# Performance work log

Hardware: AMD Instinct MI355X
Metric: run time of the kernel (lower is better)

Reference implementation:

```python
import jax, jax.numpy as jnp
import numpy as np

TEMPERATURE = 0.1
EPS = 1e-12

def _l2norm(x):
    # matches F.normalize(x, dim=-1)
    return x / jnp.maximum(jnp.linalg.norm(x, axis=-1, keepdims=True), EPS)

def setup_inputs() -> dict:
    key = jax.random.key(0)
    k1, k2 = jax.random.split(key)
    N, D = 8192, 256
    images = jax.random.normal(k1, (N, D), dtype=jnp.float32)
    captions = jax.random.normal(k2, (N, D), dtype=jnp.float32)
    return {"images": images, "captions": captions}

def reference(images, captions):
    # Batched equivalent of the per-sample loop:
    # for each image i, InfoNCE(anchor=image_i, pos=caption_i, negs=all other captions)
    # and symmetrically for each caption. InfoNCE (unpaired mode) normalizes
    # embeddings, builds logits [pos, negs]/T, and applies CE with target 0.
    # Softmax is permutation-invariant, so this equals symmetric CE on the
    # full NxN similarity matrix with diagonal targets (CLIP loss).
    im = _l2norm(images)    # [N, D]
    cap = _l2norm(captions)  # [N, D]
    logits = jnp.einsum('id,jd->ij', im, cap) / TEMPERATURE  # [N, N]
    diag = jnp.arange(images.shape[0])
    # image->caption losses (rows), caption->image losses (columns)
    loss_i2c = -jax.nn.log_softmax(logits, axis=1)[diag, diag]
    loss_c2i = -jax.nn.log_softmax(logits, axis=0)[diag, diag]
    # original returns mean over the 2N concatenated per-sample losses
    return (jnp.mean(loss_i2c) + jnp.mean(loss_c2i)) * 0.5
```

## Files before the change

kernel.cpp:

```cpp
#include <hip/hip_runtime.h>
#include <hip/hip_bf16.h>

typedef short bf16x8 __attribute__((ext_vector_type(8)));
typedef float f32x4 __attribute__((ext_vector_type(4)));

typedef __attribute__((address_space(3))) void as3_void;
typedef const __attribute__((address_space(1))) void as1_void;

static constexpr int D = 256;
static constexpr float INV_T = 10.0f;

__device__ __forceinline__ ushort f2bf(float f) {
  union { float f; unsigned u; } v; v.f = f;
  unsigned r = v.u + 0x7fffu + ((v.u >> 16) & 1u);
  return (ushort)(r >> 16);
}

__global__ __launch_bounds__(256) void normalize_kernel(
    const float* __restrict__ im, const float* __restrict__ cap,
    ushort* __restrict__ imn, ushort* __restrict__ capn,
    float* __restrict__ diag, int N) {
  int tid = blockIdx.x * 256 + threadIdx.x;
  int w = tid >> 6;
  int lane = threadIdx.x & 63;
  if (w >= N) return;
  float4 vi = ((const float4*)(im + (size_t)w * D))[lane];
  float4 vc = ((const float4*)(cap + (size_t)w * D))[lane];
  float ssi = vi.x*vi.x + vi.y*vi.y + vi.z*vi.z + vi.w*vi.w;
  float ssc = vc.x*vc.x + vc.y*vc.y + vc.z*vc.z + vc.w*vc.w;
  #pragma unroll
  for (int m = 1; m < 64; m <<= 1) {
    ssi += __shfl_xor(ssi, m);
    ssc += __shfl_xor(ssc, m);
  }
  float ri = 1.0f / fmaxf(sqrtf(ssi), 1e-12f);
  float rc = 1.0f / fmaxf(sqrtf(ssc), 1e-12f);
  float ax = vi.x*ri, ay = vi.y*ri, az = vi.z*ri, aw = vi.w*ri;
  float cx = vc.x*rc, cy = vc.y*rc, cz = vc.z*rc, cw = vc.w*rc;
  ushort4 ua, uc;
  ua.x = f2bf(ax); ua.y = f2bf(ay); ua.z = f2bf(az); ua.w = f2bf(aw);
  uc.x = f2bf(cx); uc.y = f2bf(cy); uc.z = f2bf(cz); uc.w = f2bf(cw);
  ((ushort4*)(imn + (size_t)w * D))[lane] = ua;
  ((ushort4*)(capn + (size_t)w * D))[lane] = uc;
  float d = ax*cx + ay*cy + az*cz + aw*cw;
  #pragma unroll
  for (int m = 1; m < 64; m <<= 1) d += __shfl_xor(d, m);
  if (lane == 0) diag[w] = d * INV_T;
}

__global__ __launch_bounds__(512) void gemm_exp_kernel(
    const ushort* __restrict__ A, const ushort* __restrict__ Bm,
    float* __restrict__ rowpart, float* __restrict__ colpart, int N) {
  __shared__ ushort As[8][128 * 32];
  __shared__ ushort Bsh[8][2][64 * 32];
  int bm = blockIdx.x >> 2;
  int cg = blockIdx.x & 3;
  int tid = threadIdx.x;
  int lane = tid & 63;
  int wv = tid >> 6;
  int rb = lane & 15;
  int kb = (lane >> 4) * 8;
  int cc = kb ^ (((rb >> 1) & 3) * 8);

  int arow = tid >> 2;
  int ascol = 8 * ((tid & 3) ^ ((tid >> 3) & 3));
  const ushort* agS = A + ((size_t)bm * 128 + arow) * D + ascol;

  int su = 8 * ((lane & 3) ^ ((lane >> 3) & 3));
  const ushort* bgS = Bm + ((size_t)(wv * 64 + (lane >> 2))) * D + su;

  f32x4 acc[8][4];

#define VMWAIT(n) asm volatile("s_waitcnt vmcnt(" #n ")" ::: "memory")
#define LGKM0() asm volatile("s_waitcnt lgkmcnt(0)" ::: "memory")
#define BARRIER() asm volatile("s_barrier" ::: "memory")

#define STAGE_A(c)                                                           \
  __builtin_amdgcn_global_load_lds((as1_void*)(agS + (c) * 32),              \
      (as3_void*)(&As[c][tid * 8]), 16, 0, 0);

#define STAGE_B(P, T, KT) {                                                  \
    const ushort* bp = bgS + (size_t)(T) * 512 * D + (KT) * 32;              \
    _Pragma("unroll")                                                        \
    for (int i = 0; i < 4; ++i)                                              \
      __builtin_amdgcn_global_load_lds(                                      \
          (as1_void*)(bp + (size_t)i * 16 * D),                              \
          (as3_void*)(&Bsh[wv][P][i * 512 + lane * 8]), 16, 0, 0);           \
  }

#define READ_A(AF, KT)                                                      \
  { _Pragma("unroll") for (int mi = 0; mi < 8; ++mi)                        \
      AF[mi] = *(const bf16x8*)(&As[KT][(mi * 16 + rb) * 32 + cc]); }

#define READ_B(BF, P)                                                       \
  { _Pragma("unroll") for (int ni = 0; ni < 4; ++ni)                        \
      BF[ni] = *(const bf16x8*)(&Bsh[wv][P][(ni * 16 + rb) * 32 + cc]); }

#define MFMAS(AF, FB, CZ)                                                   \
  { __builtin_amdgcn_s_setprio(1);                                          \
    _Pragma("unroll") for (int mi = 0; mi < 8; ++mi)                        \
      _Pragma("unroll") for (int ni = 0; ni < 4; ++ni)                      \
        acc[mi][ni] = __builtin_amdgcn_mfma_f32_16x16x32_bf16(              \
            AF[mi], FB[ni],                                                 \
            (CZ) ? (f32x4){0.f, 0.f, 0.f, 0.f} : acc[mi][ni], 0, 0, 0);     \
    __builtin_amdgcn_s_setprio(0); }

#define EPILOGUE(T) {                                                         \
    _Pragma("unroll")                                                         \
    for (int mi = 0; mi < 8; ++mi)                                            \
      _Pragma("unroll")                                                       \
      for (int ni = 0; ni < 4; ++ni)                                          \
        _Pragma("unroll")                                                     \
        for (int r = 0; r < 4; ++r)                                           \
          acc[mi][ni][r] = __expf(acc[mi][ni][r] * INV_T);                    \
    bool sb0 = (lane & 1) != 0, sb1 = (lane & 2) != 0;                        \
    _Pragma("unroll")                                                         \
    for (int mi = 0; mi < 8; ++mi) {                                          \
      float v0 = acc[mi][0][0] + acc[mi][1][0] + acc[mi][2][0] + acc[mi][3][0]; \
      float v1 = acc[mi][0][1] + acc[mi][1][1] + acc[mi][2][1] + acc[mi][3][1]; \
      float v2 = acc[mi][0][2] + acc[mi][1][2] + acc[mi][2][2] + acc[mi][3][2]; \
      float v3 = acc[mi][0][3] + acc[mi][1][3] + acc[mi][2][3] + acc[mi][3][3]; \
      float h0 = (sb0 ? v1 : v0) + __shfl_xor(sb0 ? v0 : v1, 1);              \
      float h1 = (sb0 ? v3 : v2) + __shfl_xor(sb0 ? v2 : v3, 1);              \
      float g  = (sb1 ? h1 : h0) + __shfl_xor(sb1 ? h0 : h1, 2);              \
      g += __shfl_xor(g, 4);                                                  \
      g += __shfl_xor(g, 8);                                                  \
      if ((lane & 12) == 0)                                                   \
        rowpart[(size_t)((T) * 8 + wv) * N + bm * 128 + mi * 16 +             \
                (lane >> 4) * 4 + (lane & 3)] = g;                            \
    }                                                                         \
    _Pragma("unroll")                                                         \
    for (int ni = 0; ni < 4; ++ni) {                                          \
      float v = 0.f;                                                          \
      _Pragma("unroll")                                                       \
      for (int mi = 0; mi < 8; ++mi)                                          \
        _Pragma("unroll")                                                     \
        for (int r = 0; r < 4; ++r)                                           \
          v += acc[mi][ni][r];                                                \
      v += __shfl_xor(v, 16); v += __shfl_xor(v, 32);                         \
      if (lane < 16)                                                          \
        colpart[(size_t)bm * N + (T) * 512 + wv * 64 + ni * 16 + lane] = v;   \
    }                                                                         \
  }

  int T0 = cg * 4;
  STAGE_A(0) STAGE_A(1) STAGE_A(2) STAGE_A(3)
  STAGE_A(4) STAGE_A(5) STAGE_A(6) STAGE_A(7)
  STAGE_B(0, T0, 0)
  STAGE_B(1, T0, 1)
  VMWAIT(8);
  BARRIER();
  VMWAIT(4);
  bf16x8 fbA[4], fbB[4];
  READ_B(fbA, 0)

  for (int j = 0; j < 4; ++j) {
    int T = cg * 4 + j;
    bf16x8 af[8];
    LGKM0();
    READ_A(af, 0)
    if (j > 0) { VMWAIT(0); }
    STAGE_B(0, T, 2)
    if (j == 0) { VMWAIT(4); }
    READ_B(fbB, 1)
    MFMAS(af, fbA, 1)
    LGKM0(); STAGE_B(1, T, 3) READ_A(af, 1) VMWAIT(4); READ_B(fbA, 0)
    MFMAS(af, fbB, 0)
    LGKM0(); STAGE_B(0, T, 4) READ_A(af, 2) VMWAIT(4); READ_B(fbB, 1)
    MFMAS(af, fbA, 0)
    LGKM0(); STAGE_B(1, T, 5) READ_A(af, 3) VMWAIT(4); READ_B(fbA, 0)
    MFMAS(af, fbB, 0)
    LGKM0(); STAGE_B(0, T, 6) READ_A(af, 4) VMWAIT(4); READ_B(fbB, 1)
    MFMAS(af, fbA, 0)
    LGKM0(); STAGE_B(1, T, 7) READ_A(af, 5) VMWAIT(4); READ_B(fbA, 0)
    MFMAS(af, fbB, 0)
    LGKM0();
    if (j < 3) { STAGE_B(0, T + 1, 0) READ_A(af, 6) VMWAIT(4); }
    else       { READ_A(af, 6) VMWAIT(0); }
    READ_B(fbB, 1)
    MFMAS(af, fbA, 0)
    LGKM0();
    if (j < 3) { STAGE_B(1, T + 1, 1) READ_A(af, 7) VMWAIT(4); READ_B(fbA, 0) }
    else       { READ_A(af, 7) }
    MFMAS(af, fbB, 0)
    EPILOGUE(T)
  }
  VMWAIT(0);

#undef EPILOGUE
#undef MFMAS
#undef READ_B
#undef READ_A
#undef STAGE_B
#undef STAGE_A
#undef VMWAIT
#undef LGKM0
#undef BARRIER
}

__global__ __launch_bounds__(256) void reduce_kernel(
    const float* __restrict__ rowpart, const float* __restrict__ colpart,
    const float* __restrict__ diag, float* __restrict__ out,
    int N, int NPr, int NPc) {
  __shared__ float redr[4][64], redc[4][64];
  int w = threadIdx.x >> 6, s = threadIdx.x & 63;
  int i = blockIdx.x * 64 + s;
  float rs = 0.f, cs = 0.f;
  for (int k = w; k < NPr; k += 4) rs += rowpart[(size_t)k * N + i];
  for (int k = w; k < NPc; k += 4) cs += colpart[(size_t)k * N + i];
  redr[w][s] = rs; redc[w][s] = cs;
  __syncthreads();
  if (w == 0) {
    float R = redr[0][s] + redr[1][s] + redr[2][s] + redr[3][s];
    float C = redc[0][s] + redc[1][s] + redc[2][s] + redc[3][s];
    float l = logf(R) + logf(C) - 2.0f * diag[i];
    #pragma unroll
    for (int m = 1; m < 64; m <<= 1) l += __shfl_xor(l, m);
    if (s == 0) atomicAdd(out, l * (0.5f / (float)N));
  }
}

extern "C" void kernel_launch(void* const* d_in, const int* in_sizes, int n_in,
                              void* d_out, int out_size, void* d_ws, size_t ws_size,
                              hipStream_t stream) {
  const float* images = (const float*)d_in[0];
  const float* captions = (const float*)d_in[1];
  int N = in_sizes[0] / D;
  int NPr = 128;
  int NPc = 64;
  char* w = (char*)d_ws;
  size_t off = 0;
  ushort* imn  = (ushort*)(w + off); off += (size_t)N * D * 2;
  ushort* capn = (ushort*)(w + off); off += (size_t)N * D * 2;
  float* diag    = (float*)(w + off); off += (size_t)N * 4;
  float* rowpart = (float*)(w + off); off += (size_t)NPr * N * 4;
  float* colpart = (float*)(w + off); off += (size_t)NPc * N * 4;
  float* out = (float*)d_out;

  normalize_kernel<<<N / 4, 256, 0, stream>>>(images, captions, imn, capn, diag, N);
  gemm_exp_kernel<<<256, 512, 0, stream>>>(imn, capn, rowpart, colpart, N);
  hipMemsetAsync(out, 0, sizeof(float), stream);
  reduce_kernel<<<N / 64, 256, 0, stream>>>(rowpart, colpart, diag, out, N, NPr, NPc);
}
```

Measured before the change: 68.28 us.

## Shrink GEMM block tile to 64 rows and double grid for two blocks per CU

Halves the per-block A tile (128 to 64 rows) and per-wave B tile (64 to 32 columns), cutting accumulators from 32 to 8 MFMA tiles. Doubles the grid to 512 blocks with launch_bounds(512,2) so two blocks can co-reside per CU, which should hide latency better. The partial-sum buffers grow (256 row partials, 128 column partials), adding reduce work. Smaller tiles lower data reuse per MFMA, so LDS and global traffic per flop rises.

After: 82.61 us. 1.21x slower.

```diff
diff --git a/kernel.cpp b/kernel.cpp
--- a/kernel.cpp
+++ b/kernel.cpp
@@ -48,11 +48,11 @@
   if (lane == 0) diag[w] = d * INV_T;
 }
 
-__global__ __launch_bounds__(512) void gemm_exp_kernel(
+__global__ __launch_bounds__(512, 2) void gemm_exp_kernel(
     const ushort* __restrict__ A, const ushort* __restrict__ Bm,
     float* __restrict__ rowpart, float* __restrict__ colpart, int N) {
-  __shared__ ushort As[8][128 * 32];
-  __shared__ ushort Bsh[8][2][64 * 32];
+  __shared__ ushort As[8][64 * 32];
+  __shared__ ushort Bsh[8][2][32 * 32];
   int bm = blockIdx.x >> 2;
   int cg = blockIdx.x & 3;
   int tid = threadIdx.x;
@@ -62,44 +62,48 @@
   int kb = (lane >> 4) * 8;
   int cc = kb ^ (((rb >> 1) & 3) * 8);
 
-  int arow = tid >> 2;
-  int ascol = 8 * ((tid & 3) ^ ((tid >> 3) & 3));
-  const ushort* agS = A + ((size_t)bm * 128 + arow) * D + ascol;
+  int inner = tid & 255;
+  int chalf = tid >> 8;
+  int ar = inner >> 2;
+  int asu = 8 * ((inner & 3) ^ ((inner >> 3) & 3));
+  const ushort* agS = A + ((size_t)bm * 64 + ar) * D + asu;
 
   int su = 8 * ((lane & 3) ^ ((lane >> 3) & 3));
-  const ushort* bgS = Bm + ((size_t)(wv * 64 + (lane >> 2))) * D + su;
-
-  f32x4 acc[8][4];
+
+  f32x4 acc[4][2];
 
 #define VMWAIT(n) asm volatile("s_waitcnt vmcnt(" #n ")" ::: "memory")
 #define LGKM0() asm volatile("s_waitcnt lgkmcnt(0)" ::: "memory")
 #define BARRIER() asm volatile("s_barrier" ::: "memory")
 
-#define STAGE_A(c)                                                           \
-  __builtin_amdgcn_global_load_lds((as1_void*)(agS + (c) * 32),              \
-      (as3_void*)(&As[c][tid * 8]), 16, 0, 0);
+#define STAGE_A(r) {                                                         \
+    int c_ = chalf * 4 + (r);                                                \
+    __builtin_amdgcn_global_load_lds((as1_void*)(agS + c_ * 32),             \
+        (as3_void*)(&As[0][0] + c_ * 2048 + inner * 8), 16, 0, 0);           \
+  }
 
 #define STAGE_B(P, T, KT) {                                                  \
-    const ushort* bp = bgS + (size_t)(T) * 512 * D + (KT) * 32;              \
-    _Pragma("unroll")                                                        \
-    for (int i = 0; i < 4; ++i)                                              \
-      __builtin_amdgcn_global_load_lds(                                      \
-          (as1_void*)(bp + (size_t)i * 16 * D),                              \
-          (as3_void*)(&Bsh[wv][P][i * 512 + lane * 8]), 16, 0, 0);           \
+    const ushort* bp = Bm +                                                  \
+        ((size_t)(cg * 2048 + (T) * 256 + wv * 32 + (lane >> 2))) * D +      \
+        su + (KT) * 32;                                                      \
+    __builtin_amdgcn_global_load_lds((as1_void*)(bp),                        \
+        (as3_void*)(&Bsh[wv][P][lane * 8]), 16, 0, 0);                       \
+    __builtin_amdgcn_global_load_lds((as1_void*)(bp + (size_t)16 * D),       \
+        (as3_void*)(&Bsh[wv][P][512 + lane * 8]), 16, 0, 0);                 \
   }
 
 #define READ_A(AF, KT)                                                      \
-  { _Pragma("unroll") for (int mi = 0; mi < 8; ++mi)                        \
+  { _Pragma("unroll") for (int mi = 0; mi < 4; ++mi)                        \
       AF[mi] = *(const bf16x8*)(&As[KT][(mi * 16 + rb) * 32 + cc]); }
 
 #define READ_B(BF, P)                                                       \
-  { _Pragma("unroll") for (int ni = 0; ni < 4; ++ni)                        \
+  { _Pragma("unroll") for (int ni = 0; ni < 2; ++ni)                        \
       BF[ni] = *(const bf16x8*)(&Bsh[wv][P][(ni * 16 + rb) * 32 + cc]); }
 
 #define MFMAS(AF, FB, CZ)                                                   \
   { __builtin_amdgcn_s_setprio(1);                                          \
-    _Pragma("unroll") for (int mi = 0; mi < 8; ++mi)                        \
-      _Pragma("unroll") for (int ni = 0; ni < 4; ++ni)                      \
+    _Pragma("unroll") for (int mi = 0; mi < 4; ++mi)                        \
+      _Pragma("unroll") for (int ni = 0; ni < 2; ++ni)                      \
         acc[mi][ni] = __builtin_amdgcn_mfma_f32_16x16x32_bf16(              \
             AF[mi], FB[ni],                                                 \
             (CZ) ? (f32x4){0.f, 0.f, 0.f, 0.f} : acc[mi][ni], 0, 0, 0);     \
@@ -107,83 +111,78 @@
 
 #define EPILOGUE(T) {                                                         \
     _Pragma("unroll")                                                         \
-    for (int mi = 0; mi < 8; ++mi)                                            \
+    for (int mi = 0; mi < 4; ++mi)                                            \
       _Pragma("unroll")                                                       \
-      for (int ni = 0; ni < 4; ++ni)                                          \
+      for (int ni = 0; ni < 2; ++ni)                                          \
         _Pragma("unroll")                                                     \
         for (int r = 0; r < 4; ++r)                                           \
           acc[mi][ni][r] = __expf(acc[mi][ni][r] * INV_T);                    \
     bool sb0 = (lane & 1) != 0, sb1 = (lane & 2) != 0;                        \
     _Pragma("unroll")                                                         \
-    for (int mi = 0; mi < 8; ++mi) {                                          \
-      float v0 = acc[mi][0][0] + acc[mi][1][0] + acc[mi][2][0] + acc[mi][3][0]; \
-      float v1 = acc[mi][0][1] + acc[mi][1][1] + acc[mi][2][1] + acc[mi][3][1]; \
-      float v2 = acc[mi][0][2] + acc[mi][1][2] + acc[mi][2][2] + acc[mi][3][2]; \
-      float v3 = acc[mi][0][3] + acc[mi][1][3] + acc[mi][2][3] + acc[mi][3][3]; \
+    for (int mi = 0; mi < 4; ++mi) {                                          \
+      float v0 = acc[mi][0][0] + acc[mi][1][0];                               \
+      float v1 = acc[mi][0][1] + acc[mi][1][1];                               \
+      float v2 = acc[mi][0][2] + acc[mi][1][2];                               \
+      float v3 = acc[mi][0][3] + acc[mi][1][3];                               \
       float h0 = (sb0 ? v1 : v0) + __shfl_xor(sb0 ? v0 : v1, 1);              \
       float h1 = (sb0 ? v3 : v2) + __shfl_xor(sb0 ? v2 : v3, 1);              \
       float g  = (sb1 ? h1 : h0) + __shfl_xor(sb1 ? h0 : h1, 2);              \
       g += __shfl_xor(g, 4);                                                  \
       g += __shfl_xor(g, 8);                                                  \
       if ((lane & 12) == 0)                                                   \
-        rowpart[(size_t)((T) * 8 + wv) * N + bm * 128 + mi * 16 +             \
+        rowpart[(size_t)(cg * 64 + (T) * 8 + wv) * N + bm * 64 + mi * 16 +    \
                 (lane >> 4) * 4 + (lane & 3)] = g;                            \
     }                                                                         \
     _Pragma("unroll")                                                         \
-    for (int ni = 0; ni < 4; ++ni) {                                          \
+    for (int ni = 0; ni < 2; ++ni) {                                          \
       float v = 0.f;                                                          \
       _Pragma("unroll")                                                       \
-      for (int mi = 0; mi < 8; ++mi)                                          \
+      for (int mi = 0; mi < 4; ++mi)                                          \
         _Pragma("unroll")                                                     \
         for (int r = 0; r < 4; ++r)                                           \
           v += acc[mi][ni][r];                                                \
       v += __shfl_xor(v, 16); v += __shfl_xor(v, 32);                         \
       if (lane < 16)                                                          \
-        colpart[(size_t)bm * N + (T) * 512 + wv * 64 + ni * 16 + lane] = v;   \
+        colpart[(size_t)bm * N + cg * 2048 + (T) * 256 + wv * 32 + ni * 16 +  \
+                lane] = v;                                                    \
     }                                                                         \
   }
 
-  int T0 = cg * 4;
   STAGE_A(0) STAGE_A(1) STAGE_A(2) STAGE_A(3)
-  STAGE_A(4) STAGE_A(5) STAGE_A(6) STAGE_A(7)
-  STAGE_B(0, T0, 0)
-  STAGE_B(1, T0, 1)
-  VMWAIT(8);
+  STAGE_B(0, 0, 0)
+  STAGE_B(1, 0, 1)
+  VMWAIT(4);
   BARRIER();
-  VMWAIT(4);
-  bf16x8 fbA[4], fbB[4];
+  VMWAIT(2);
+  bf16x8 fbA[2], fbB[2];
   READ_B(fbA, 0)
 
-  for (int j = 0; j < 4; ++j) {
-    int T = cg * 4 + j;
-    bf16x8 af[8];
+  for (int T = 0; T < 8; ++T) {
+    bf16x8 af[4];
+    LGKM0(); STAGE_B(0, T, 2) READ_A(af, 0) VMWAIT(2); READ_B(fbB, 1)
+    MFMAS(af, fbA, 1)
+    LGKM0(); STAGE_B(1, T, 3) READ_A(af, 1) VMWAIT(2); READ_B(fbA, 0)
+    MFMAS(af, fbB, 0)
+    LGKM0(); STAGE_B(0, T, 4) READ_A(af, 2) VMWAIT(2); READ_B(fbB, 1)
+    MFMAS(af, fbA, 0)
+    LGKM0(); STAGE_B(1, T, 5) READ_A(af, 3) VMWAIT(2); READ_B(fbA, 0)
+    MFMAS(af, fbB, 0)
+    LGKM0(); STAGE_B(0, T, 6) READ_A(af, 4) VMWAIT(2); READ_B(fbB, 1)
+    MFMAS(af, fbA, 0)
+    LGKM0(); STAGE_B(1, T, 7) READ_A(af, 5) VMWAIT(2); READ_B(fbA, 0)
+    MFMAS(af, fbB, 0)
     LGKM0();
-    READ_A(af, 0)
-    if (j > 0) { VMWAIT(0); }
-    STAGE_B(0, T, 2)
-    if (j == 0) { VMWAIT(4); }
-    READ_B(fbB, 1)
-    MFMAS(af, fbA, 1)
-    LGKM0(); STAGE_B(1, T, 3) READ_A(af, 1) VMWAIT(4); READ_B(fbA, 0)
-    MFMAS(af, fbB, 0)
-    LGKM0(); STAGE_B(0, T, 4) READ_A(af, 2) VMWAIT(4); READ_B(fbB, 1)
-    MFMAS(af, fbA, 0)
-    LGKM0(); STAGE_B(1, T, 5) READ_A(af, 3) VMWAIT(4); READ_B(fbA, 0)
-    MFMAS(af, fbB, 0)
-    LGKM0(); STAGE_B(0, T, 6) READ_A(af, 4) VMWAIT(4); READ_B(fbB, 1)
-    MFMAS(af, fbA, 0)
-    LGKM0(); STAGE_B(1, T, 7) READ_A(af, 5) VMWAIT(4); READ_B(fbA, 0)
-    MFMAS(af, fbB, 0)
-    LGKM0();
-    if (j < 3) { STAGE_B(0, T + 1, 0) READ_A(af, 6) VMWAIT(4); }
+    if (T < 7) { STAGE_B(0, T + 1, 0) READ_A(af, 6) VMWAIT(2); }
     else       { READ_A(af, 6) VMWAIT(0); }
     READ_B(fbB, 1)
     MFMAS(af, fbA, 0)
     LGKM0();
-    if (j < 3) { STAGE_B(1, T + 1, 1) READ_A(af, 7) VMWAIT(4); READ_B(fbA, 0) }
-    else       { READ_A(af, 7) }
-    MFMAS(af, fbB, 0)
+    if (T < 7) { STAGE_B(1, T + 1, 1) }
+    READ_A(af, 7)
+    MFMAS(af, fbB, 0)
+    VMWAIT(0);
     EPILOGUE(T)
+    READ_B(fbA, 0)
   }
   VMWAIT(0);
 
@@ -226,8 +225,8 @@
   const float* images = (const float*)d_in[0];
   const float* captions = (const float*)d_in[1];
   int N = in_sizes[0] / D;
-  int NPr = 128;
-  int NPc = 64;
+  int NPr = 256;
+  int NPc = 128;
   char* w = (char*)d_ws;
   size_t off = 0;
   ushort* imn  = (ushort*)(w + off); off += (size_t)N * D * 2;
@@ -238,7 +237,7 @@
   float* out = (float*)d_out;
 
   normalize_kernel<<<N / 4, 256, 0, stream>>>(images, captions, imn, capn, diag, N);
-  gemm_exp_kernel<<<256, 512, 0, stream>>>(imn, capn, rowpart, colpart, N);
+  gemm_exp_kernel<<<512, 512, 0, stream>>>(imn, capn, rowpart, colpart, N);
   hipMemsetAsync(out, 0, sizeof(float), stream);
   reduce_kernel<<<N / 64, 256, 0, stream>>>(rowpart, colpart, diag, out, N, NPr, NPc);
 }
```
